# Performance work log

Measured on AMD Instinct MI355X. Metric: run time of the kernel, lower is better.

The kernel has to match this reference:

```python
import jax, jax.numpy as jnp
import numpy as np

B, V, K, C = 32, 65536, 8, 3


def setup_inputs() -> dict:
    key = jax.random.key(0)
    k1, k2, k3, k4 = jax.random.split(key, 4)
    out = jax.random.normal(k1, (B, V, C), dtype=jnp.float32)
    tgt = jax.random.normal(k2, (B, V, C), dtype=jnp.float32)
    neighbor_idxs = jax.random.randint(k3, (V, K), 0, V, dtype=jnp.int32)
    # Laplacian weights: each row sums to -1 (lap = x - weighted mean of neighbors)
    w = jax.random.uniform(k4, (V, K), dtype=jnp.float32) + 1e-3
    neighbor_weights = -w / jnp.sum(w, axis=-1, keepdims=True)
    return {
        "out": out,
        "tgt": tgt,
        "neighbor_idxs": neighbor_idxs,
        "neighbor_weights": neighbor_weights,
    }


def _compute_laplacian(x, neighbor_idxs, neighbor_weights):
    # x: [B, V, C]; gather -> [B, V, K, C]; weighted sum over K; residual add
    gathered = x[:, neighbor_idxs]                       # [B, V, K, C]
    return x + jnp.sum(gathered * neighbor_weights[None, :, :, None], axis=2)


def reference(out, tgt, neighbor_idxs, neighbor_weights):
    lap_out = _compute_laplacian(out, neighbor_idxs, neighbor_weights)
    lap_tgt = _compute_laplacian(tgt, neighbor_idxs, neighbor_weights)
    return (lap_out - lap_tgt) ** 2
```

## Files before the change

kernel.cpp:

```cpp
#include <hip/hip_runtime.h>

#define BB 32
#define VV 65536
#define KK 8
#define CC 3

constexpr int TV   = 64;
constexpr int ROW  = BB * CC;
constexpr int PROW = ROW + 1;
constexpr int TILE_ELEMS = TV * ROW;

__global__ __launch_bounds__(256) void lap_pass1_transpose_sub(
    const float* __restrict__ outp, const float* __restrict__ tgtp,
    float* __restrict__ dt) {
  __shared__ float tile[TV * PROW];
  const int t  = threadIdx.x;
  const int v0 = blockIdx.x * TV;

  const float4* o4 = (const float4*)outp;
  const float4* t4 = (const float4*)tgtp;
  const int src_base4 = (v0 * CC) >> 2;
  #pragma unroll
  for (int l4 = t; l4 < TILE_ELEMS / 4; l4 += 256) {
    int b  = l4 / (TV * CC / 4);
    int j4 = l4 - b * (TV * CC / 4);
    int src = b * (VV * CC / 4) + src_base4 + j4;
    float4 a = o4[src];
    float4 g = t4[src];
    float dv[4] = {a.x - g.x, a.y - g.y, a.z - g.z, a.w - g.w};
    int j = 4 * j4;
    #pragma unroll
    for (int q = 0; q < 4; q++) {
      int jj = j + q;
      int vrel = jj / CC, c = jj - vrel * CC;
      tile[vrel * PROW + b * CC + c] = dv[q];
    }
  }
  __syncthreads();

  float4* dst4 = (float4*)(dt + v0 * ROW);
  #pragma unroll
  for (int l4 = t; l4 < TILE_ELEMS / 4; l4 += 256) {
    int e = 4 * l4;
    int vrel = e / ROW, r = e - vrel * ROW;
    const float* p = &tile[vrel * PROW + r];
    dst4[l4] = make_float4(p[0], p[1], p[2], p[3]);
  }
}

__global__ __launch_bounds__(256) void lap_pass2_gather(
    const float* __restrict__ dt, const int* __restrict__ nidx,
    const float* __restrict__ nw, float* __restrict__ res) {
  __shared__ float rtile[TV * PROW];
  __shared__ int   idx_s[TV * KK];
  __shared__ float w_s[TV * KK];
  const int t  = threadIdx.x;
  const int v0 = blockIdx.x * TV;

  #pragma unroll
  for (int l = t; l < TV * KK; l += 256) {
    idx_s[l] = nidx[v0 * KK + l];
    w_s[l]   = nw[v0 * KK + l];
  }
  __syncthreads();

  const int g    = t >> 5;
  const int lane = t & 31;
  #pragma unroll
  for (int i = 0; i < TV / 8; i++) {
    const int vrel = i * 8 + g;
    const int v    = v0 + vrel;
    const float* self = dt + v * ROW + lane * CC;
    float ax = self[0], ay = self[1], az = self[2];
    #pragma unroll
    for (int k = 0; k < KK; k++) {
      const int   nb = idx_s[vrel * KK + k];
      const float wt = w_s[vrel * KK + k];
      const float* p = dt + nb * ROW + lane * CC;
      ax = fmaf(wt, p[0], ax);
      ay = fmaf(wt, p[1], ay);
      az = fmaf(wt, p[2], az);
    }
    float* rp = &rtile[vrel * PROW + lane * CC];
    rp[0] = ax * ax; rp[1] = ay * ay; rp[2] = az * az;
  }
  __syncthreads();

  float4* r4 = (float4*)res;
  const int dst_base4 = (v0 * CC) >> 2;
  #pragma unroll
  for (int l4 = t; l4 < TILE_ELEMS / 4; l4 += 256) {
    int b  = l4 / (TV * CC / 4);
    int j4 = l4 - b * (TV * CC / 4);
    int j  = 4 * j4;
    float tmp[4];
    #pragma unroll
    for (int q = 0; q < 4; q++) {
      int jj = j + q;
      int vrel = jj / CC, c = jj - vrel * CC;
      tmp[q] = rtile[vrel * PROW + b * CC + c];
    }
    r4[b * (VV * CC / 4) + dst_base4 + j4] = make_float4(tmp[0], tmp[1], tmp[2], tmp[3]);
  }
}

__global__ __launch_bounds__(256) void lap_fused_fallback(
    const float* __restrict__ outp, const float* __restrict__ tgtp,
    const int* __restrict__ nidx, const float* __restrict__ nw,
    float* __restrict__ res) {
  int tid = blockIdx.x * 256 + threadIdx.x;
  if (tid >= BB * VV) return;
  int v = tid & (VV - 1);
  int b = tid >> 16;
  float ax = 0.f, ay = 0.f, az = 0.f;
  #pragma unroll
  for (int k = 0; k < KK; k++) {
    int   nb = nidx[v * KK + k];
    float wt = nw[v * KK + k];
    const float* po = outp + (b * VV + nb) * CC;
    const float* pt = tgtp + (b * VV + nb) * CC;
    ax = fmaf(wt, po[0] - pt[0], ax);
    ay = fmaf(wt, po[1] - pt[1], ay);
    az = fmaf(wt, po[2] - pt[2], az);
  }
  const float* so = outp + tid * CC;
  const float* st = tgtp + tid * CC;
  float dx = so[0] - st[0] + ax;
  float dy = so[1] - st[1] + ay;
  float dz = so[2] - st[2] + az;
  float* rp = res + tid * CC;
  rp[0] = dx * dx; rp[1] = dy * dy; rp[2] = dz * dz;
}

extern "C" void kernel_launch(void* const* d_in, const int* in_sizes, int n_in,
                              void* d_out, int out_size, void* d_ws, size_t ws_size,
                              hipStream_t stream) {
  const float* outp = (const float*)d_in[0];
  const float* tgtp = (const float*)d_in[1];
  const int*   nidx = (const int*)d_in[2];
  const float* nw   = (const float*)d_in[3];
  float* res = (float*)d_out;

  const size_t dt_bytes = (size_t)VV * ROW * sizeof(float);
  if (ws_size >= dt_bytes) {
    float* dt = (float*)d_ws;
    lap_pass1_transpose_sub<<<VV / TV, 256, 0, stream>>>(outp, tgtp, dt);
    lap_pass2_gather<<<VV / TV, 256, 0, stream>>>(dt, nidx, nw, res);
  } else {
    lap_fused_fallback<<<(BB * VV) / 256, 256, 0, stream>>>(outp, tgtp, nidx, nw, res);
  }
}
```

Baseline: 128.9 us.

## Store transposed difference workspace in bf16 to halve gather traffic

The first pass now rounds the out-minus-target differences to bf16 and packs two per 32-bit word. This halves the workspace footprint and the bytes the second pass gathers per neighbor. The gather kernel remaps threads so each lane handles two batch entries (six channels), reads vectorized neighbor indices and weights from LDS, and unpacks bf16 to fp32 before accumulating. The cost is reduced precision in the intermediate differences, which may exceed output tolerance.

```diff
diff --git a/kernel.cpp b/kernel.cpp
--- a/kernel.cpp
+++ b/kernel.cpp
@@ -9,10 +9,19 @@
 constexpr int ROW  = BB * CC;
 constexpr int PROW = ROW + 1;
 constexpr int TILE_ELEMS = TV * ROW;
+constexpr int ROWU = ROW / 2;
+
+__device__ __forceinline__ unsigned int f2bf(float f) {
+  unsigned int u = __float_as_uint(f);
+  u += 0x7FFFu + ((u >> 16) & 1u);
+  return u >> 16;
+}
+__device__ __forceinline__ float bflo(unsigned int u) { return __uint_as_float(u << 16); }
+__device__ __forceinline__ float bfhi(unsigned int u) { return __uint_as_float(u & 0xFFFF0000u); }
 
 __global__ __launch_bounds__(256) void lap_pass1_transpose_sub(
     const float* __restrict__ outp, const float* __restrict__ tgtp,
-    float* __restrict__ dt) {
+    unsigned int* __restrict__ dt) {
   __shared__ float tile[TV * PROW];
   const int t  = threadIdx.x;
   const int v0 = blockIdx.x * TV;
@@ -38,18 +47,23 @@
   }
   __syncthreads();
 
-  float4* dst4 = (float4*)(dt + v0 * ROW);
+  uint4* dst = (uint4*)(dt + (size_t)v0 * ROWU);
   #pragma unroll
-  for (int l4 = t; l4 < TILE_ELEMS / 4; l4 += 256) {
-    int e = 4 * l4;
+  for (int i8 = t; i8 < TILE_ELEMS / 8; i8 += 256) {
+    int e = i8 * 8;
     int vrel = e / ROW, r = e - vrel * ROW;
     const float* p = &tile[vrel * PROW + r];
-    dst4[l4] = make_float4(p[0], p[1], p[2], p[3]);
+    uint4 o;
+    o.x = f2bf(p[0]) | (f2bf(p[1]) << 16);
+    o.y = f2bf(p[2]) | (f2bf(p[3]) << 16);
+    o.z = f2bf(p[4]) | (f2bf(p[5]) << 16);
+    o.w = f2bf(p[6]) | (f2bf(p[7]) << 16);
+    dst[i8] = o;
   }
 }
 
 __global__ __launch_bounds__(256) void lap_pass2_gather(
-    const float* __restrict__ dt, const int* __restrict__ nidx,
+    const unsigned int* __restrict__ dt, const int* __restrict__ nidx,
     const float* __restrict__ nw, float* __restrict__ res) {
   __shared__ float rtile[TV * PROW];
   __shared__ int   idx_s[TV * KK];
@@ -57,32 +71,46 @@
   const int t  = threadIdx.x;
   const int v0 = blockIdx.x * TV;
 
-  #pragma unroll
   for (int l = t; l < TV * KK; l += 256) {
     idx_s[l] = nidx[v0 * KK + l];
     w_s[l]   = nw[v0 * KK + l];
   }
   __syncthreads();
 
-  const int g    = t >> 5;
-  const int lane = t & 31;
-  #pragma unroll
-  for (int i = 0; i < TV / 8; i++) {
-    const int vrel = i * 8 + g;
+  const int g = t >> 4;
+  const int l = t & 15;
+  #pragma unroll 2
+  for (int i = 0; i < TV / 16; i++) {
+    const int vrel = i * 16 + g;
     const int v    = v0 + vrel;
-    const float* self = dt + v * ROW + lane * CC;
-    float ax = self[0], ay = self[1], az = self[2];
+
+    const int4*   ip = (const int4*)&idx_s[vrel * KK];
+    const float4* wp = (const float4*)&w_s[vrel * KK];
+    int4   ia = ip[0], ib = ip[1];
+    float4 wa = wp[0], wb = wp[1];
+    int   nbk[KK] = {ia.x, ia.y, ia.z, ia.w, ib.x, ib.y, ib.z, ib.w};
+    float wk[KK]  = {wa.x, wa.y, wa.z, wa.w, wb.x, wb.y, wb.z, wb.w};
+
+    const unsigned int* sp = dt + (size_t)v * ROWU + 3 * l;
+    unsigned int s0 = sp[0], s1 = sp[1], s2 = sp[2];
+    float x0 = bflo(s0), y0 = bfhi(s0), z0 = bflo(s1);
+    float x1 = bfhi(s1), y1 = bflo(s2), z1 = bfhi(s2);
+
     #pragma unroll
     for (int k = 0; k < KK; k++) {
-      const int   nb = idx_s[vrel * KK + k];
-      const float wt = w_s[vrel * KK + k];
-      const float* p = dt + nb * ROW + lane * CC;
-      ax = fmaf(wt, p[0], ax);
-      ay = fmaf(wt, p[1], ay);
-      az = fmaf(wt, p[2], az);
+      const unsigned int* p = dt + (size_t)nbk[k] * ROWU + 3 * l;
+      unsigned int u0 = p[0], u1 = p[1], u2 = p[2];
+      const float wt = wk[k];
+      x0 = fmaf(wt, bflo(u0), x0);
+      y0 = fmaf(wt, bfhi(u0), y0);
+      z0 = fmaf(wt, bflo(u1), z0);
+      x1 = fmaf(wt, bfhi(u1), x1);
+      y1 = fmaf(wt, bflo(u2), y1);
+      z1 = fmaf(wt, bfhi(u2), z1);
     }
-    float* rp = &rtile[vrel * PROW + lane * CC];
-    rp[0] = ax * ax; rp[1] = ay * ay; rp[2] = az * az;
+    float* rp = &rtile[vrel * PROW + 6 * l];
+    rp[0] = x0 * x0; rp[1] = y0 * y0; rp[2] = z0 * z0;
+    rp[3] = x1 * x1; rp[4] = y1 * y1; rp[5] = z1 * z1;
   }
   __syncthreads();
 
@@ -117,18 +145,18 @@
   for (int k = 0; k < KK; k++) {
     int   nb = nidx[v * KK + k];
     float wt = nw[v * KK + k];
-    const float* po = outp + (b * VV + nb) * CC;
-    const float* pt = tgtp + (b * VV + nb) * CC;
+    const float* po = outp + ((size_t)b * VV + nb) * CC;
+    const float* pt = tgtp + ((size_t)b * VV + nb) * CC;
     ax = fmaf(wt, po[0] - pt[0], ax);
     ay = fmaf(wt, po[1] - pt[1], ay);
     az = fmaf(wt, po[2] - pt[2], az);
   }
-  const float* so = outp + tid * CC;
-  const float* st = tgtp + tid * CC;
+  const float* so = outp + (size_t)tid * CC;
+  const float* st = tgtp + (size_t)tid * CC;
   float dx = so[0] - st[0] + ax;
   float dy = so[1] - st[1] + ay;
   float dz = so[2] - st[2] + az;
-  float* rp = res + tid * CC;
+  float* rp = res + (size_t)tid * CC;
   rp[0] = dx * dx; rp[1] = dy * dy; rp[2] = dz * dz;
 }
 
@@ -141,9 +169,9 @@
   const float* nw   = (const float*)d_in[3];
   float* res = (float*)d_out;
 
-  const size_t dt_bytes = (size_t)VV * ROW * sizeof(float);
+  const size_t dt_bytes = (size_t)VV * ROW * 2;
   if (ws_size >= dt_bytes) {
-    float* dt = (float*)d_ws;
+    unsigned int* dt = (unsigned int*)d_ws;
     lap_pass1_transpose_sub<<<VV / TV, 256, 0, stream>>>(outp, tgtp, dt);
     lap_pass2_gather<<<VV / TV, 256, 0, stream>>>(dt, nidx, nw, res);
   } else {
```

After: 114.2 us, median of 2. 11.5% less time.
